# Kernel tuning notes

Hardware: AMD Instinct MI355X
Metric: run time of the kernel (lower is better)

Reference implementation:

```python
import jax, jax.numpy as jnp
import numpy as np

LAMBDA_COORD = 5.0
LAMBDA_NOOBJ = 0.5
NUM_CLASSES = 80


def setup_inputs() -> dict:
    key = jax.random.key(0)
    k1, k2 = jax.random.split(key)
    B, G, C5, T = 64, 80, NUM_CLASSES + 5, 50
    predictions = jax.random.normal(k1, (B, G, G, C5), dtype=jnp.float32)
    t = jax.random.uniform(k2, (B, T, 5), dtype=jnp.float32)  # coords in [0,1)
    # col 0 holds the class id as a float (cast with .long() in the original)
    targets = t.at[..., 0].set(jnp.floor(t[..., 0] * NUM_CLASSES))
    return {"predictions": predictions, "targets": targets}


def reference(predictions, targets):
    B, G, _, C5 = predictions.shape
    T = targets.shape[1]
    nc = C5 - 5

    cls_id = targets[..., 0].astype(jnp.int32)              # (B,T)
    xg = targets[..., 1] * G
    yg = targets[..., 2] * G
    wg = targets[..., 3] * G
    hg = targets[..., 4] * G

    # obj/coord/class path clamps the cell index (int() truncation == floor for >=0)
    gx = jnp.clip(xg.astype(jnp.int32), 0, G - 1)           # (B,T)
    gy = jnp.clip(yg.astype(jnp.int32), 0, G - 1)
    bidx = jnp.broadcast_to(jnp.arange(B)[:, None], (B, T))
    pred = predictions[bidx, gy, gx]                         # (B,T,C5) gather of responsible cells

    sp = jax.nn.softplus
    # BCEWithLogits(z, 1) = softplus(-z), summed over all targets
    obj_loss = sp(-pred[..., 0]).sum()

    x_t = xg - gx.astype(xg.dtype)
    y_t = yg - gy.astype(yg.dtype)
    coord_loss = LAMBDA_COORD * (
        ((jax.nn.sigmoid(pred[..., 1]) - x_t) ** 2).sum()
        + ((jax.nn.sigmoid(pred[..., 2]) - y_t) ** 2).sum()
        + ((pred[..., 3] - wg) ** 2).sum()
        + ((pred[..., 4] - hg) ** 2).sum()
    )

    # BCEWithLogits(z, onehot) summed = sum softplus(z) - z * t
    z = pred[..., 5:]                                        # (B,T,nc)
    onehot = jax.nn.one_hot(cls_id, nc, dtype=z.dtype)
    class_loss = (sp(z) - z * onehot).sum()

    # noobj path uses the UNclamped truncated index (coords in [0,1) so identical here)
    tx = xg.astype(jnp.int32)
    ty = yg.astype(jnp.int32)
    occupied = jnp.zeros((B, G, G), dtype=bool).at[bidx, ty, tx].set(True)
    noobj_loss = LAMBDA_NOOBJ * jnp.where(
        occupied, jnp.float32(0.0), sp(predictions[..., 0])
    ).sum()

    Bf = jnp.float32(B)
    obj_loss = obj_loss / Bf
    noobj_loss = noobj_loss / Bf
    coord_loss = coord_loss / Bf
    class_loss = class_loss / Bf
    total = obj_loss + noobj_loss + coord_loss + class_loss
    return total, obj_loss, noobj_loss, coord_loss, class_loss
```

## Files before the change

### kernel.cpp

```cpp
#include <hip/hip_runtime.h>
#include <math.h>

#define GRID_SZ 80
#define NT      50
#define C5      85
#define BATCH   64
#define TPB     320
#define CELLS   (GRID_SZ*GRID_SZ)
#define CPB     640
#define BPI     10
#define NBLK    (BATCH*BPI)
#define NSLOT   (NBLK*4)
#define MAGIC   0x5A17C0DEu

__device__ __forceinline__ float sp(float x) {
    return fmaxf(x, 0.0f) + __logf(1.0f + __expf(-fabsf(x)));
}


__global__ __launch_bounds__(TPB) void fused_kernel(const float* __restrict__ pred,
                                                    const float* __restrict__ tgt,
                                                    unsigned long long* __restrict__ slots,
                                                    float* __restrict__ out) {
    const int tid  = threadIdx.x;
    const int lane = tid & 63;
    const int w    = tid >> 6;
    const int b    = blockIdx.x / BPI;
    const int blk  = blockIdx.x % BPI;

    const size_t cellbase = (size_t)b * CELLS + blk * CPB;
    const float p0a = pred[(cellbase + tid)       * C5];
    const float p0b = pred[(cellbase + tid + TPB) * C5];

    __shared__ unsigned s_bits[CPB / 32];
    __shared__ float    s_red[5][4];

    if (tid < CPB / 32) s_bits[tid] = 0u;
    __syncthreads();

    if (tid < NT) {
        const float* tp = tgt + ((size_t)b * NT + tid) * 5;
        const int tx = (int)(tp[1] * GRID_SZ);
        const int ty = (int)(tp[2] * GRID_SZ);
        const int c  = ty * GRID_SZ + tx - blk * CPB;
        if ((unsigned)c < CPB) atomicOr(&s_bits[c >> 5], 1u << (c & 31));
    }

    float obj = 0.f, coord = 0.f, cls = 0.f;
    {
        const int gt = blockIdx.x * 5 + w;
        const int tb = gt / NT, tt = gt - tb * NT;
        const float* tp = tgt + ((size_t)tb * NT + tt) * 5;
        const float t0 = tp[0], t1 = tp[1], t2 = tp[2], t3 = tp[3], t4 = tp[4];
        const int   cid = (int)t0;
        const float xg = t1 * GRID_SZ, yg = t2 * GRID_SZ;
        const float wg = t3 * GRID_SZ, hg = t4 * GRID_SZ;
        const int gx = min(max((int)xg, 0), GRID_SZ - 1);
        const int gy = min(max((int)yg, 0), GRID_SZ - 1);
        const float xt = xg - (float)gx;
        const float yt = yg - (float)gy;
        const float* pp = pred + (((size_t)tb * GRID_SZ + gy) * GRID_SZ + gx) * C5;

        {
            const float p = pp[lane];
            if (lane == 0)      obj = sp(-p);
            else if (lane == 1) { const float s = 1.f / (1.f + __expf(-p)); const float d = s - xt; coord = d * d; }
            else if (lane == 2) { const float s = 1.f / (1.f + __expf(-p)); const float d = s - yt; coord = d * d; }
            else if (lane == 3) { const float d = p - wg; coord = d * d; }
            else if (lane == 4) { const float d = p - hg; coord = d * d; }
            else                cls = sp(p) - ((lane - 5) == cid ? p : 0.f);
        }
        const int c2 = lane + 64;
        if (c2 < C5) {
            const float p = pp[c2];
            cls += sp(p) - ((c2 - 5) == cid ? p : 0.f);
        }
    }

    __syncthreads();
    const bool occA = (s_bits[tid >> 5]        >> (tid & 31)) & 1u;
    const bool occB = (s_bits[(tid >> 5) + 10] >> (tid & 31)) & 1u;
    float nob = (occA ? 0.f : sp(p0a)) + (occB ? 0.f : sp(p0b));

    #pragma unroll
    for (int off = 32; off; off >>= 1) {
        obj   += __shfl_xor(obj,   off);
        coord += __shfl_xor(coord, off);
        cls   += __shfl_xor(cls,   off);
        nob   += __shfl_xor(nob,   off);
    }
    if (lane == 0) { s_red[w][0] = obj; s_red[w][1] = coord; s_red[w][2] = cls; s_red[w][3] = nob; }
    __syncthreads();
    if (tid < 4) {
        const float v = s_red[0][tid] + s_red[1][tid] + s_red[2][tid] + s_red[3][tid] + s_red[4][tid];
        const unsigned u = __float_as_uint(v);
        const unsigned long long pk =
            (unsigned long long)u | ((unsigned long long)(u ^ MAGIC) << 32);
        __hip_atomic_store(&slots[(size_t)blockIdx.x * 4 + tid], pk,
                           __ATOMIC_RELAXED, __HIP_MEMORY_SCOPE_AGENT);
    }

    if (blockIdx.x == 0) {
        unsigned long long v[8];
        bool ok;
        do {
            ok = true;
            #pragma unroll
            for (int j = 0; j < 8; ++j)
                v[j] = __hip_atomic_load(&slots[tid + j * TPB],
                                         __ATOMIC_RELAXED, __HIP_MEMORY_SCOPE_AGENT);
            #pragma unroll
            for (int j = 0; j < 8; ++j)
                ok &= ((unsigned)(v[j] >> 32) == (((unsigned)v[j]) ^ MAGIC));
        } while (!ok);
        float acc = 0.f;
        #pragma unroll
        for (int j = 0; j < 8; ++j) acc += __uint_as_float((unsigned)v[j]);

        #pragma unroll
        for (int off = 4; off <= 32; off <<= 1) acc += __shfl_xor(acc, off);

        __shared__ float s_fin[5][4];
        if (lane < 4) s_fin[w][lane] = acc;
        __syncthreads();
        if (tid == 0) {
            float sums[4];
            #pragma unroll
            for (int c = 0; c < 4; ++c)
                sums[c] = s_fin[0][c] + s_fin[1][c] + s_fin[2][c] + s_fin[3][c] + s_fin[4][c];
            const float invB   = 1.f / (float)BATCH;
            const float objT   = sums[0] * invB;
            const float coordT = 5.0f * sums[1] * invB;
            const float clsT   = sums[2] * invB;
            const float nobT   = 0.5f * sums[3] * invB;
            out[0] = objT + nobT + coordT + clsT;
            out[1] = objT;
            out[2] = nobT;
            out[3] = coordT;
            out[4] = clsT;
        }
    }
}

extern "C" void kernel_launch(void* const* d_in, const int* in_sizes, int n_in,
                              void* d_out, int out_size, void* d_ws, size_t ws_size,
                              hipStream_t stream) {
    const float* pred = (const float*)d_in[0];
    const float* tgt  = (const float*)d_in[1];
    unsigned long long* slots = (unsigned long long*)d_ws;
    float* out = (float*)d_out;

    fused_kernel<<<NBLK, TPB, 0, stream>>>(pred, tgt, slots, out);
}
```

Baseline: 15.93 us.

## Compute noobj as full sum minus deduplicated occupied cells in extra blocks

Each gather block now sums softplus over all of its confidence cells, without building a shared-memory occupancy bitmap and without the associated syncthreads. Sixty-four extra blocks, one per image, deduplicate that image's target cells with wave shuffles and subtract softplus for each unique occupied cell. The final reducer in block 0 reads 704*4 slots, so some threads load a ninth slot. This takes a barrier and the atomics off the main path, but it adds blocks and a subtraction that can lose float precision.

```diff
diff --git a/kernel.cpp b/kernel.cpp
--- a/kernel.cpp
+++ b/kernel.cpp
@@ -9,7 +9,8 @@
 #define CELLS   (GRID_SZ*GRID_SZ)
 #define CPB     640
 #define BPI     10
-#define NBLK    (BATCH*BPI)
+#define NGATHER (BATCH*BPI)
+#define NBLK    (NGATHER + BATCH)
 #define NSLOT   (NBLK*4)
 #define MAGIC   0x5A17C0DEu
 
@@ -25,62 +26,69 @@
     const int tid  = threadIdx.x;
     const int lane = tid & 63;
     const int w    = tid >> 6;
-    const int b    = blockIdx.x / BPI;
-    const int blk  = blockIdx.x % BPI;
 
-    const size_t cellbase = (size_t)b * CELLS + blk * CPB;
-    const float p0a = pred[(cellbase + tid)       * C5];
-    const float p0b = pred[(cellbase + tid + TPB) * C5];
+    float obj = 0.f, coord = 0.f, cls = 0.f, nob = 0.f;
 
-    __shared__ unsigned s_bits[CPB / 32];
-    __shared__ float    s_red[5][4];
+    if (blockIdx.x < NGATHER) {
+        const int b   = blockIdx.x / BPI;
+        const int blk = blockIdx.x % BPI;
 
-    if (tid < CPB / 32) s_bits[tid] = 0u;
-    __syncthreads();
-
-    if (tid < NT) {
-        const float* tp = tgt + ((size_t)b * NT + tid) * 5;
-        const int tx = (int)(tp[1] * GRID_SZ);
-        const int ty = (int)(tp[2] * GRID_SZ);
-        const int c  = ty * GRID_SZ + tx - blk * CPB;
-        if ((unsigned)c < CPB) atomicOr(&s_bits[c >> 5], 1u << (c & 31));
-    }
-
-    float obj = 0.f, coord = 0.f, cls = 0.f;
-    {
-        const int gt = blockIdx.x * 5 + w;
-        const int tb = gt / NT, tt = gt - tb * NT;
-        const float* tp = tgt + ((size_t)tb * NT + tt) * 5;
-        const float t0 = tp[0], t1 = tp[1], t2 = tp[2], t3 = tp[3], t4 = tp[4];
-        const int   cid = (int)t0;
-        const float xg = t1 * GRID_SZ, yg = t2 * GRID_SZ;
-        const float wg = t3 * GRID_SZ, hg = t4 * GRID_SZ;
-        const int gx = min(max((int)xg, 0), GRID_SZ - 1);
-        const int gy = min(max((int)yg, 0), GRID_SZ - 1);
-        const float xt = xg - (float)gx;
-        const float yt = yg - (float)gy;
-        const float* pp = pred + (((size_t)tb * GRID_SZ + gy) * GRID_SZ + gx) * C5;
+        const size_t cellbase = (size_t)b * CELLS + blk * CPB;
+        const float p0a = pred[(cellbase + tid)       * C5];
+        const float p0b = pred[(cellbase + tid + TPB) * C5];
 
         {
-            const float p = pp[lane];
-            if (lane == 0)      obj = sp(-p);
-            else if (lane == 1) { const float s = 1.f / (1.f + __expf(-p)); const float d = s - xt; coord = d * d; }
-            else if (lane == 2) { const float s = 1.f / (1.f + __expf(-p)); const float d = s - yt; coord = d * d; }
-            else if (lane == 3) { const float d = p - wg; coord = d * d; }
-            else if (lane == 4) { const float d = p - hg; coord = d * d; }
-            else                cls = sp(p) - ((lane - 5) == cid ? p : 0.f);
+            const int gt = blockIdx.x * 5 + w;
+            const int tb = gt / NT, tt = gt - tb * NT;
+            const float* tp = tgt + ((size_t)tb * NT + tt) * 5;
+            const float t0 = tp[0], t1 = tp[1], t2 = tp[2], t3 = tp[3], t4 = tp[4];
+            const int   cid = (int)t0;
+            const float xg = t1 * GRID_SZ, yg = t2 * GRID_SZ;
+            const float wg = t3 * GRID_SZ, hg = t4 * GRID_SZ;
+            const int gx = min(max((int)xg, 0), GRID_SZ - 1);
+            const int gy = min(max((int)yg, 0), GRID_SZ - 1);
+            const float xt = xg - (float)gx;
+            const float yt = yg - (float)gy;
+            const float* pp = pred + (((size_t)tb * GRID_SZ + gy) * GRID_SZ + gx) * C5;
+
+            {
+                const float p = pp[lane];
+                if (lane == 0)      obj = sp(-p);
+                else if (lane == 1) { const float s = 1.f / (1.f + __expf(-p)); const float d = s - xt; coord = d * d; }
+                else if (lane == 2) { const float s = 1.f / (1.f + __expf(-p)); const float d = s - yt; coord = d * d; }
+                else if (lane == 3) { const float d = p - wg; coord = d * d; }
+                else if (lane == 4) { const float d = p - hg; coord = d * d; }
+                else                cls = sp(p) - ((lane - 5) == cid ? p : 0.f);
+            }
+            const int c2 = lane + 64;
+            if (c2 < C5) {
+                const float p = pp[c2];
+                cls += sp(p) - ((c2 - 5) == cid ? p : 0.f);
+            }
         }
-        const int c2 = lane + 64;
-        if (c2 < C5) {
-            const float p = pp[c2];
-            cls += sp(p) - ((c2 - 5) == cid ? p : 0.f);
+
+        nob = sp(p0a) + sp(p0b);
+    } else {
+        const int img = blockIdx.x - NGATHER;
+        if (w == 0) {
+            const int t = lane;
+            int cell = -1 - t;
+            if (t < NT) {
+                const float* tp = tgt + ((size_t)img * NT + t) * 5;
+                const int tx = (int)(tp[1] * GRID_SZ);
+                const int ty = (int)(tp[2] * GRID_SZ);
+                cell = ty * GRID_SZ + tx;
+            }
+            bool first = (t < NT);
+            #pragma unroll
+            for (int u = 0; u < NT; ++u) {
+                const int cu = __shfl(cell, u);
+                first &= !((u < t) && (cu == cell));
+            }
+            if (first)
+                nob = -sp(pred[((size_t)img * CELLS + cell) * C5]);
         }
     }
-
-    __syncthreads();
-    const bool occA = (s_bits[tid >> 5]        >> (tid & 31)) & 1u;
-    const bool occB = (s_bits[(tid >> 5) + 10] >> (tid & 31)) & 1u;
-    float nob = (occA ? 0.f : sp(p0a)) + (occB ? 0.f : sp(p0b));
 
     #pragma unroll
     for (int off = 32; off; off >>= 1) {
@@ -89,10 +97,12 @@
         cls   += __shfl_xor(cls,   off);
         nob   += __shfl_xor(nob,   off);
     }
+    __shared__ float s_red[5][4];
     if (lane == 0) { s_red[w][0] = obj; s_red[w][1] = coord; s_red[w][2] = cls; s_red[w][3] = nob; }
     __syncthreads();
     if (tid < 4) {
-        const float v = s_red[0][tid] + s_red[1][tid] + s_red[2][tid] + s_red[3][tid] + s_red[4][tid];
+        const float v = s_red[0][tid] + s_red[1][tid] + s_red[2][tid]
+                      + s_red[3][tid] + s_red[4][tid];
         const unsigned u = __float_as_uint(v);
         const unsigned long long pk =
             (unsigned long long)u | ((unsigned long long)(u ^ MAGIC) << 32);
@@ -101,7 +111,8 @@
     }
 
     if (blockIdx.x == 0) {
-        unsigned long long v[8];
+        const bool has9 = (tid < 256);
+        unsigned long long v[9];
         bool ok;
         do {
             ok = true;
@@ -109,13 +120,19 @@
             for (int j = 0; j < 8; ++j)
                 v[j] = __hip_atomic_load(&slots[tid + j * TPB],
                                          __ATOMIC_RELAXED, __HIP_MEMORY_SCOPE_AGENT);
+            if (has9)
+                v[8] = __hip_atomic_load(&slots[tid + 8 * TPB],
+                                         __ATOMIC_RELAXED, __HIP_MEMORY_SCOPE_AGENT);
             #pragma unroll
             for (int j = 0; j < 8; ++j)
                 ok &= ((unsigned)(v[j] >> 32) == (((unsigned)v[j]) ^ MAGIC));
+            if (has9)
+                ok &= ((unsigned)(v[8] >> 32) == (((unsigned)v[8]) ^ MAGIC));
         } while (!ok);
         float acc = 0.f;
         #pragma unroll
         for (int j = 0; j < 8; ++j) acc += __uint_as_float((unsigned)v[j]);
+        if (has9) acc += __uint_as_float((unsigned)v[8]);
 
         #pragma unroll
         for (int off = 4; off <= 32; off <<= 1) acc += __shfl_xor(acc, off);
@@ -127,7 +144,8 @@
             float sums[4];
             #pragma unroll
             for (int c = 0; c < 4; ++c)
-                sums[c] = s_fin[0][c] + s_fin[1][c] + s_fin[2][c] + s_fin[3][c] + s_fin[4][c];
+                sums[c] = s_fin[0][c] + s_fin[1][c] + s_fin[2][c]
+                        + s_fin[3][c] + s_fin[4][c];
             const float invB   = 1.f / (float)BATCH;
             const float objT   = sums[0] * invB;
             const float coordT = 5.0f * sums[1] * invB;
```

Result: faster. 15.51 us, median of 2 (-2.6%).
